# Kernel tuning notes

Measured on AMD Instinct MI355X. Metric: run time of the kernel, lower is better.

Reference implementation:

```python
import jax, jax.numpy as jnp
import numpy as np

N_, CIN, H_, W_ = 2, 128, 240, 320
C_, HEADS, WS, DEPTH, HID, DOUT, NQ = 128, 4, 7, 4, 512, 256, 128

def _ln(x, g, b, eps=1e-5):
    mu = x.mean(-1, keepdims=True)
    var = ((x - mu) ** 2).mean(-1, keepdims=True)
    return (x - mu) / jnp.sqrt(var + eps) * g + b

def setup_inputs() -> dict:
    key = jax.random.key(0)
    ks = jax.random.split(key, 16)
    s = 0.02
    d = {}
    d['x'] = jax.random.normal(ks[0], (N_, CIN, H_, W_), jnp.float32)
    d['conv_w'] = jax.random.normal(ks[1], (C_, CIN), jnp.float32) * s
    d['conv_b'] = jnp.zeros((C_,), jnp.float32)
    d['n1_g'] = jnp.ones((DEPTH, C_), jnp.float32)
    d['n1_b'] = jnp.zeros((DEPTH, C_), jnp.float32)
    d['qkv_w'] = jax.random.normal(ks[2], (DEPTH, 3 * C_, C_), jnp.float32) * s
    d['qkv_b'] = jnp.zeros((DEPTH, 3 * C_), jnp.float32)
    d['proj_w'] = jax.random.normal(ks[3], (DEPTH, C_, C_), jnp.float32) * s
    d['proj_b'] = jnp.zeros((DEPTH, C_), jnp.float32)
    d['n2_g'] = jnp.ones((DEPTH, C_), jnp.float32)
    d['n2_b'] = jnp.zeros((DEPTH, C_), jnp.float32)
    d['fc1_w'] = jax.random.normal(ks[4], (DEPTH, HID, C_), jnp.float32) * s
    d['fc1_b'] = jnp.zeros((DEPTH, HID), jnp.float32)
    d['fc2_w'] = jax.random.normal(ks[5], (DEPTH, C_, HID), jnp.float32) * s
    d['fc2_b'] = jnp.zeros((DEPTH, C_), jnp.float32)
    d['r1_w'] = jax.random.normal(ks[6], (256, C_), jnp.float32) * s
    d['r1_b'] = jnp.zeros((256,), jnp.float32)
    d['r2_w'] = jax.random.normal(ks[7], (256, 256), jnp.float32) * s
    d['r2_b'] = jnp.zeros((256,), jnp.float32)
    d['r3_w'] = jax.random.normal(ks[8], (DOUT, 256), jnp.float32) * s
    d['r3_b'] = jnp.zeros((DOUT,), jnp.float32)
    return d

def _block(t, H, W, n1_g, n1_b, qkv_w, qkv_b, proj_w, proj_b, n2_g, n2_b, fc1_w, fc1_b, fc2_w, fc2_b):
    N, L, C = t.shape
    hd = C // HEADS
    scale = hd ** -0.5
    shortcut = t
    h = _ln(t, n1_g, n1_b).reshape(N, H, W, C)
    pad_h = (-H) % WS
    pad_w = (-W) % WS
    h = jnp.pad(h, ((0, 0), (0, pad_h), (0, pad_w), (0, 0)))
    Hp, Wp = H + pad_h, W + pad_w
    # partition into (num_windows*N, ws*ws, C)
    h = h.reshape(N, Hp // WS, WS, Wp // WS, WS, C).transpose(0, 1, 3, 2, 4, 5).reshape(-1, WS * WS, C)
    B_ = h.shape[0]
    qkv = (h @ qkv_w.T + qkv_b).reshape(B_, WS * WS, 3, HEADS, hd).transpose(2, 0, 3, 1, 4)
    q, k, v = qkv[0], qkv[1], qkv[2]
    attn = jax.nn.softmax(jnp.einsum('bhqd,bhkd->bhqk', q, k) * scale, axis=-1)
    o = jnp.einsum('bhqk,bhkd->bhqd', attn, v).transpose(0, 2, 1, 3).reshape(B_, WS * WS, C)
    o = o @ proj_w.T + proj_b
    # reverse window partition
    o = o.reshape(N, Hp // WS, Wp // WS, WS, WS, C).transpose(0, 1, 3, 2, 4, 5).reshape(N, Hp, Wp, C)[:, :H, :W, :].reshape(N, H * W, C)
    t = shortcut + o
    h2 = _ln(t, n2_g, n2_b)
    m = jax.nn.gelu(h2 @ fc1_w.T + fc1_b, approximate=False) @ fc2_w.T + fc2_b
    return t + m

def reference(x, conv_w, conv_b, n1_g, n1_b, qkv_w, qkv_b, proj_w, proj_b, n2_g, n2_b, fc1_w, fc1_b, fc2_w, fc2_b, r1_w, r1_b, r2_w, r2_b, r3_w, r3_b):
    N, Cin, H, W = x.shape
    xp = jnp.einsum('nchw,ec->nehw', x, conv_w) + conv_b[None, :, None, None]  # (N,C,H,W)
    tokens = xp.reshape(N, C_, H * W).transpose(0, 2, 1)  # (N,HW,C)
    for i in range(DEPTH):
        tokens = _block(tokens, H, W, n1_g[i], n1_b[i], qkv_w[i], qkv_b[i], proj_w[i], proj_b[i], n2_g[i], n2_b[i], fc1_w[i], fc1_b[i], fc2_w[i], fc2_b[i])
    head = tokens.mean(axis=1)  # (N,C)
    queries = tokens[:, :NQ, :]  # (N,NQ,C)
    maps = jnp.einsum('nchw,nqc->nqhw', xp, queries)  # PixelWiseDotProduct
    y = jax.nn.leaky_relu(head @ r1_w.T + r1_b, 0.01)
    y = jax.nn.leaky_relu(y @ r2_w.T + r2_b, 0.01)
    y = y @ r3_w.T + r3_b
    y = jax.nn.relu(y) + 0.1  # norm == 'linear'
    y = y / y.sum(axis=1, keepdims=True)
    return (y, maps)
```

## Files before the change

### kernel.cpp

```cpp
#include <hip/hip_runtime.h>
#include <hip/hip_bf16.h>

typedef __hip_bfloat16 bf16;

static constexpr int Nn = 2, CIN = 128, Hh = 240, Ww = 320, HW = 76800;
static constexpr int Cc = 128, HID = 512, DOUT = 256, WSQ = 49;
static constexpr int NWH = 35, NWW = 46, WPN = NWH * NWW;
static constexpr int NWIN = Nn * WPN;
static constexpr float SCALE = 0.17677669529663687f;

typedef __attribute__((ext_vector_type(8))) short s8;
typedef __attribute__((ext_vector_type(4))) short s4;
typedef __attribute__((ext_vector_type(2))) short s2;
typedef __attribute__((ext_vector_type(4))) float f4;

__device__ __forceinline__ short f2bf(float x) {
  union { bf16 b; short s; } u; u.b = __float2bfloat16(x); return u.s;
}

#define MFMA(a, b, c) __builtin_amdgcn_mfma_f32_16x16x32_bf16((a), (b), (c), 0, 0, 0)

__global__ __launch_bounds__(256) void cast_bf16(const float* __restrict__ src,
                                                 short* __restrict__ dst, int n) {
  const int i = (blockIdx.x * 256 + threadIdx.x) * 4;
  if (i < n) {
    const float4 v = *(const float4*)(src + i);
    s4 o; o[0] = f2bf(v.x); o[1] = f2bf(v.y); o[2] = f2bf(v.z); o[3] = f2bf(v.w);
    *(s4*)(dst + i) = o;
  }
}

__global__ void init_head(float* headbuf) {
  if (threadIdx.x < 256) headbuf[threadIdx.x] = 0.f;
}

__global__ __launch_bounds__(256) void conv_kernel(
    const float* __restrict__ x, const float* __restrict__ conv_w, const float* __restrict__ conv_b,
    float* __restrict__ tok) {
  __shared__ float wlds[128 * 128];
  const int tid = threadIdx.x;
  for (int idx = tid; idx < 16384; idx += 256) {
    const int e = idx & 127, c = idx >> 7;
    wlds[c * 128 + e] = conv_w[e * 128 + c];
  }
  __syncthreads();
  const int n = blockIdx.y;
  const int hw0 = blockIdx.x * 128;
  const int hwi = tid & 63, eg = tid >> 6;
  const float* xn = x + (size_t)n * CIN * HW + hw0 + hwi;
  float acc0[32], acc1[32];
#pragma unroll
  for (int jj = 0; jj < 32; jj++) {
    const float b = conv_b[eg * 32 + jj];
    acc0[jj] = b; acc1[jj] = b;
  }
  for (int c = 0; c < CIN; c++) {
    const float xv0 = xn[(size_t)c * HW];
    const float xv1 = xn[(size_t)c * HW + 64];
    const float* wl = wlds + c * 128 + eg * 32;
#pragma unroll
    for (int jj = 0; jj < 8; jj++) {
      const float4 w4 = *(const float4*)(wl + jj * 4);
      acc0[jj*4+0] = fmaf(w4.x, xv0, acc0[jj*4+0]); acc1[jj*4+0] = fmaf(w4.x, xv1, acc1[jj*4+0]);
      acc0[jj*4+1] = fmaf(w4.y, xv0, acc0[jj*4+1]); acc1[jj*4+1] = fmaf(w4.y, xv1, acc1[jj*4+1]);
      acc0[jj*4+2] = fmaf(w4.z, xv0, acc0[jj*4+2]); acc1[jj*4+2] = fmaf(w4.z, xv1, acc1[jj*4+2]);
      acc0[jj*4+3] = fmaf(w4.w, xv0, acc0[jj*4+3]); acc1[jj*4+3] = fmaf(w4.w, xv1, acc1[jj*4+3]);
    }
  }
  float* tb0 = tok + ((size_t)n * HW + hw0 + hwi) * Cc + eg * 32;
  float* tb1 = tb0 + (size_t)64 * Cc;
#pragma unroll
  for (int jj = 0; jj < 8; jj++) {
    *(float4*)(tb0 + jj * 4) = make_float4(acc0[jj*4], acc0[jj*4+1], acc0[jj*4+2], acc0[jj*4+3]);
    *(float4*)(tb1 + jj * 4) = make_float4(acc1[jj*4], acc1[jj*4+1], acc1[jj*4+2], acc1[jj*4+3]);
  }
}

__global__ __launch_bounds__(256, 2) void attn_kernel(
    float* __restrict__ tok,
    const float* __restrict__ n1_g, const float* __restrict__ n1_b,
    const short* __restrict__ wqkv, const float* __restrict__ qkv_b,
    const short* __restrict__ wproj, const float* __restrict__ proj_b,
    int layer) {
  __shared__ __align__(16) short xwv[9216];
  __shared__ __align__(16) short qkp[4][5120];

  const int tid = threadIdx.x;
  const int w = tid >> 6, lane = tid & 63;
  const int lq = lane >> 4, li = lane & 15;
  const int wi = blockIdx.x;
  const int n = wi / WPN;
  const int r0 = wi % WPN;
  const int wh = r0 / NWW, ww = r0 % NWW;

  const short* wqkv_l = wqkv + (size_t)layer * 384 * 128;
  const short* wproj_l = wproj + (size_t)layer * 128 * 128;

  for (int ti = w; ti < WSQ; ti += 4) {
    const int hh = wh * 7 + ti / 7, wv = ww * 7 + ti % 7;
    const bool valid = (hh < Hh) && (wv < Ww);
    float2 v = make_float2(0.f, 0.f);
    if (valid) v = *(const float2*)(tok + ((size_t)n * HW + hh * Ww + wv) * Cc + 2 * lane);
    float s = v.x + v.y, q = v.x * v.x + v.y * v.y;
#pragma unroll
    for (int m = 1; m < 64; m <<= 1) { s += __shfl_xor(s, m); q += __shfl_xor(q, m); }
    const float mean = s * (1.f / 128.f);
    const float rstd = rsqrtf(fmaxf(q * (1.f / 128.f) - mean * mean, 0.f) + 1e-5f);
    const int c = 2 * lane;
    float o0 = 0.f, o1 = 0.f;
    if (valid) {
      o0 = (v.x - mean) * rstd * n1_g[layer * Cc + c]     + n1_b[layer * Cc + c];
      o1 = (v.y - mean) * rstd * n1_g[layer * Cc + c + 1] + n1_b[layer * Cc + c + 1];
    }
    s2 pk; pk[0] = f2bf(o0); pk[1] = f2bf(o1);
    *(s2*)(xwv + ti * 136 + c) = pk;
  }
  for (int idx = tid; idx < 15 * 136; idx += 256) {
    xwv[(49 + idx / 136) * 136 + (idx % 136)] = 0;
  }
  __syncthreads();

  {
    const int n0 = 64 * w;
    f4 acc[4][4];
#pragma unroll
    for (int mt = 0; mt < 4; mt++)
#pragma unroll
      for (int nt = 0; nt < 4; nt++) acc[mt][nt] = f4{0.f, 0.f, 0.f, 0.f};
    for (int s = 0; s < 4; s++) {
      s8 a[4], b[4];
#pragma unroll
      for (int mt = 0; mt < 4; mt++)
        a[mt] = *(const s8*)(wqkv_l + (n0 + mt * 16 + li) * 128 + s * 32 + lq * 8);
#pragma unroll
      for (int nt = 0; nt < 4; nt++)
        b[nt] = *(const s8*)(xwv + (nt * 16 + li) * 136 + s * 32 + lq * 8);
#pragma unroll
      for (int mt = 0; mt < 4; mt++)
#pragma unroll
        for (int nt = 0; nt < 4; nt++) acc[mt][nt] = MFMA(a[mt], b[nt], acc[mt][nt]);
    }
    const bool isq = (w < 2);
    const float scl = isq ? SCALE : 1.f;
    const int koff = isq ? 0 : 2560;
#pragma unroll
    for (int mt = 0; mt < 4; mt++) {
      const int nbase = n0 + mt * 16 + lq * 4;
      const int hsel = (isq ? nbase : (nbase - 128)) >> 5;
      const int d0 = nbase & 31;
      const float4 bb = *(const float4*)(qkv_b + layer * 384 + nbase);
#pragma unroll
      for (int nt = 0; nt < 4; nt++) {
        const int tokn = nt * 16 + li;
        s4 pk;
        pk[0] = f2bf((acc[mt][nt][0] + bb.x) * scl);
        pk[1] = f2bf((acc[mt][nt][1] + bb.y) * scl);
        pk[2] = f2bf((acc[mt][nt][2] + bb.z) * scl);
        pk[3] = f2bf((acc[mt][nt][3] + bb.w) * scl);
        *(s4*)(qkp[hsel] + koff + tokn * 40 + d0) = pk;
      }
    }
  }

  {
    const int n0v = 32 * w;
    f4 acc2[4][2];
#pragma unroll
    for (int mt = 0; mt < 4; mt++)
#pragma unroll
      for (int nt = 0; nt < 2; nt++) acc2[mt][nt] = f4{0.f, 0.f, 0.f, 0.f};
    for (int s = 0; s < 4; s++) {
      s8 a[4], b[2];
#pragma unroll
      for (int mt = 0; mt < 4; mt++)
        a[mt] = *(const s8*)(xwv + (mt * 16 + li) * 136 + s * 32 + lq * 8);
#pragma unroll
      for (int nt = 0; nt < 2; nt++)
        b[nt] = *(const s8*)(wqkv_l + (256 + n0v + nt * 16 + li) * 128 + s * 32 + lq * 8);
#pragma unroll
      for (int mt = 0; mt < 4; mt++)
#pragma unroll
        for (int nt = 0; nt < 2; nt++) acc2[mt][nt] = MFMA(a[mt], b[nt], acc2[mt][nt]);
    }
    __syncthreads();
#pragma unroll
    for (int nt = 0; nt < 2; nt++) {
      const int d = n0v + nt * 16 + li;
      const float bv = qkv_b[layer * 384 + 256 + d];
#pragma unroll
      for (int mt = 0; mt < 4; mt++) {
        const int m0 = mt * 16 + lq * 4;
        s4 pk;
        pk[0] = f2bf(acc2[mt][nt][0] + bv);
        pk[1] = f2bf(acc2[mt][nt][1] + bv);
        pk[2] = f2bf(acc2[mt][nt][2] + bv);
        pk[3] = f2bf(acc2[mt][nt][3] + bv);
        *(s4*)(xwv + d * 72 + m0) = pk;
      }
    }
  }

  {
    short* qbase = qkp[w];
    short* kbase = qkp[w] + 2560;
    s8 ak[4], bq[4];
#pragma unroll
    for (int kt = 0; kt < 4; kt++) ak[kt] = *(const s8*)(kbase + (kt * 16 + li) * 40 + lq * 8);
#pragma unroll
    for (int qt = 0; qt < 4; qt++) bq[qt] = *(const s8*)(qbase + (qt * 16 + li) * 40 + lq * 8);
    f4 sc[4][4];
#pragma unroll
    for (int kt = 0; kt < 4; kt++)
#pragma unroll
      for (int qt = 0; qt < 4; qt++) sc[kt][qt] = f4{0.f, 0.f, 0.f, 0.f};
#pragma unroll
    for (int kt = 0; kt < 4; kt++)
#pragma unroll
      for (int qt = 0; qt < 4; qt++) sc[kt][qt] = MFMA(ak[kt], bq[qt], sc[kt][qt]);
#pragma unroll
    for (int kt = 0; kt < 4; kt++)
#pragma unroll
      for (int r = 0; r < 4; r++)
        if (kt * 16 + lq * 4 + r >= WSQ) {
#pragma unroll
          for (int qt = 0; qt < 4; qt++) sc[kt][qt][r] = -1e30f;
        }
    float inv[4];
#pragma unroll
    for (int qt = 0; qt < 4; qt++) {
      float m = -1e30f;
#pragma unroll
      for (int kt = 0; kt < 4; kt++)
#pragma unroll
        for (int r = 0; r < 4; r++) m = fmaxf(m, sc[kt][qt][r]);
      m = fmaxf(m, __shfl_xor(m, 16));
      m = fmaxf(m, __shfl_xor(m, 32));
      float ssum = 0.f;
#pragma unroll
      for (int kt = 0; kt < 4; kt++)
#pragma unroll
        for (int r = 0; r < 4; r++) {
          const float e = __expf(sc[kt][qt][r] - m);
          sc[kt][qt][r] = e; ssum += e;
        }
      ssum += __shfl_xor(ssum, 16);
      ssum += __shfl_xor(ssum, 32);
      inv[qt] = 1.f / ssum;
    }
#pragma unroll
    for (int qt = 0; qt < 4; qt++) {
      const int qq = qt * 16 + li;
#pragma unroll
      for (int kt = 0; kt < 4; kt++) {
        s4 pk;
        pk[0] = f2bf(sc[kt][qt][0] * inv[qt]);
        pk[1] = f2bf(sc[kt][qt][1] * inv[qt]);
        pk[2] = f2bf(sc[kt][qt][2] * inv[qt]);
        pk[3] = f2bf(sc[kt][qt][3] * inv[qt]);
        *(s4*)(qbase + qq * 72 + kt * 16 + lq * 4) = pk;
      }
    }
    f4 ov[2][4];
#pragma unroll
    for (int dt = 0; dt < 2; dt++)
#pragma unroll
      for (int qt = 0; qt < 4; qt++) ov[dt][qt] = f4{0.f, 0.f, 0.f, 0.f};
    for (int s = 0; s < 2; s++) {
      s8 av[2], bp[4];
#pragma unroll
      for (int dt = 0; dt < 2; dt++)
        av[dt] = *(const s8*)(xwv + (w * 32 + dt * 16 + li) * 72 + s * 32 + lq * 8);
#pragma unroll
      for (int qt = 0; qt < 4; qt++)
        bp[qt] = *(const s8*)(qbase + (qt * 16 + li) * 72 + s * 32 + lq * 8);
#pragma unroll
      for (int dt = 0; dt < 2; dt++)
#pragma unroll
        for (int qt = 0; qt < 4; qt++) ov[dt][qt] = MFMA(av[dt], bp[qt], ov[dt][qt]);
    }
    short* ohb = qkp[w] + 2560;
#pragma unroll
    for (int dt = 0; dt < 2; dt++) {
      const int dl0 = dt * 16 + lq * 4;
#pragma unroll
      for (int qt = 0; qt < 4; qt++) {
        const int tokn = qt * 16 + li;
        s4 pk;
        pk[0] = f2bf(ov[dt][qt][0]);
        pk[1] = f2bf(ov[dt][qt][1]);
        pk[2] = f2bf(ov[dt][qt][2]);
        pk[3] = f2bf(ov[dt][qt][3]);
        *(s4*)(ohb + tokn * 40 + dl0) = pk;
      }
    }
  }
  __syncthreads();

  {
    const int n0p = 32 * w;
    f4 pa[4][2];
#pragma unroll
    for (int mt = 0; mt < 4; mt++)
#pragma unroll
      for (int nt = 0; nt < 2; nt++) pa[mt][nt] = f4{0.f, 0.f, 0.f, 0.f};
    for (int s = 0; s < 4; s++) {
      s8 ao[4], bw[2];
#pragma unroll
      for (int mt = 0; mt < 4; mt++)
        ao[mt] = *(const s8*)(qkp[s] + 2560 + (mt * 16 + li) * 40 + lq * 8);
#pragma unroll
      for (int nt = 0; nt < 2; nt++)
        bw[nt] = *(const s8*)(wproj_l + (n0p + nt * 16 + li) * 128 + s * 32 + lq * 8);
#pragma unroll
      for (int mt = 0; mt < 4; mt++)
#pragma unroll
        for (int nt = 0; nt < 2; nt++) pa[mt][nt] = MFMA(ao[mt], bw[nt], pa[mt][nt]);
    }
#pragma unroll
    for (int nt = 0; nt < 2; nt++) {
      const int c = n0p + nt * 16 + li;
      const float pb = proj_b[layer * 128 + c];
#pragma unroll
      for (int mt = 0; mt < 4; mt++) {
#pragma unroll
        for (int r = 0; r < 4; r++) {
          const int m = mt * 16 + lq * 4 + r;
          if (m < WSQ) {
            const int hh = wh * 7 + m / 7, wv = ww * 7 + m % 7;
            if (hh < Hh && wv < Ww) {
              float* p = tok + ((size_t)n * HW + hh * Ww + wv) * Cc + c;
              *p += pa[mt][nt][r] + pb;
            }
          }
        }
      }
    }
  }
}

__global__ __launch_bounds__(256, 3) void mlp_kernel(
    float* __restrict__ tok,
    const float* __restrict__ n2_g, const float* __restrict__ n2_b,
    const short* __restrict__ wfc1, const float* __restrict__ fc1_b,
    const short* __restrict__ wfc2, const float* __restrict__ fc2_b,
    int layer) {
  __shared__ __align__(16) short lnb[64 * 136];
  __shared__ __align__(16) short hbuf[2][64 * 136];

  const int tid = threadIdx.x;
  const int w = tid >> 6, lane = tid & 63;
  const int lq = lane >> 4, li = lane & 15;
  const int t0 = blockIdx.x * 64;
  const short* wfc1_l = wfc1 + (size_t)layer * 512 * 128;
  const short* wfc2_l = wfc2 + (size_t)layer * 128 * 512;

#pragma unroll
  for (int i = 0; i < 16; i++) {
    const int tl = w * 16 + i;
    const float2 v = *(const float2*)(tok + (size_t)(t0 + tl) * Cc + 2 * lane);
    float s = v.x + v.y, q = v.x * v.x + v.y * v.y;
#pragma unroll
    for (int m = 1; m < 64; m <<= 1) { s += __shfl_xor(s, m); q += __shfl_xor(q, m); }
    const float mean = s * (1.f / 128.f);
    const float rstd = rsqrtf(fmaxf(q * (1.f / 128.f) - mean * mean, 0.f) + 1e-5f);
    const int c = 2 * lane;
    s2 pk;
    pk[0] = f2bf((v.x - mean) * rstd * n2_g[layer * Cc + c]     + n2_b[layer * Cc + c]);
    pk[1] = f2bf((v.y - mean) * rstd * n2_g[layer * Cc + c + 1] + n2_b[layer * Cc + c + 1]);
    *(s2*)(lnb + tl * 136 + c) = pk;
  }
  __syncthreads();

  f4 acc2[2][4];
#pragma unroll
  for (int mt = 0; mt < 2; mt++)
#pragma unroll
    for (int nt = 0; nt < 4; nt++) acc2[mt][nt] = f4{0.f, 0.f, 0.f, 0.f};
  const int c0 = 32 * w;

  for (int s = 0; s < 4; s++) {
    f4 acc1[2][4];
#pragma unroll
    for (int mt = 0; mt < 2; mt++)
#pragma unroll
      for (int nt = 0; nt < 4; nt++) acc1[mt][nt] = f4{0.f, 0.f, 0.f, 0.f};
    const int hbase = 128 * s + 32 * w;
    for (int kc = 0; kc < 4; kc++) {
      s8 a[2], b[4];
#pragma unroll
      for (int mt = 0; mt < 2; mt++)
        a[mt] = *(const s8*)(wfc1_l + (hbase + mt * 16 + li) * 128 + kc * 32 + lq * 8);
#pragma unroll
      for (int nt = 0; nt < 4; nt++)
        b[nt] = *(const s8*)(lnb + (nt * 16 + li) * 136 + kc * 32 + lq * 8);
#pragma unroll
      for (int mt = 0; mt < 2; mt++)
#pragma unroll
        for (int nt = 0; nt < 4; nt++) acc1[mt][nt] = MFMA(a[mt], b[nt], acc1[mt][nt]);
    }
    short* hb = hbuf[s & 1];
#pragma unroll
    for (int mt = 0; mt < 2; mt++) {
      const int hl0 = 32 * w + mt * 16 + lq * 4;
      const float4 bb = *(const float4*)(fc1_b + layer * HID + 128 * s + hl0);
#pragma unroll
      for (int nt = 0; nt < 4; nt++) {
        const int tokn = nt * 16 + li;
        const float g0 = acc1[mt][nt][0] + bb.x, g1 = acc1[mt][nt][1] + bb.y;
        const float g2 = acc1[mt][nt][2] + bb.z, g3 = acc1[mt][nt][3] + bb.w;
        s4 pk;
        pk[0] = f2bf(0.5f * g0 * (1.f + erff(g0 * 0.70710678118654752f)));
        pk[1] = f2bf(0.5f * g1 * (1.f + erff(g1 * 0.70710678118654752f)));
        pk[2] = f2bf(0.5f * g2 * (1.f + erff(g2 * 0.70710678118654752f)));
        pk[3] = f2bf(0.5f * g3 * (1.f + erff(g3 * 0.70710678118654752f)));
        *(s4*)(hb + tokn * 136 + hl0) = pk;
      }
    }
    __syncthreads();
    for (int kc = 0; kc < 4; kc++) {
      s8 a[2], b[4];
#pragma unroll
      for (int mt = 0; mt < 2; mt++)
        a[mt] = *(const s8*)(wfc2_l + (c0 + mt * 16 + li) * 512 + s * 128 + kc * 32 + lq * 8);
#pragma unroll
      for (int nt = 0; nt < 4; nt++)
        b[nt] = *(const s8*)(hb + (nt * 16 + li) * 136 + kc * 32 + lq * 8);
#pragma unroll
      for (int mt = 0; mt < 2; mt++)
#pragma unroll
        for (int nt = 0; nt < 4; nt++) acc2[mt][nt] = MFMA(a[mt], b[nt], acc2[mt][nt]);
    }
  }

#pragma unroll
  for (int mt = 0; mt < 2; mt++) {
    const int cb = c0 + mt * 16 + lq * 4;
    const float4 bb = *(const float4*)(fc2_b + layer * Cc + cb);
#pragma unroll
    for (int nt = 0; nt < 4; nt++) {
      const int tokn = nt * 16 + li;
      float* p = tok + (size_t)(t0 + tokn) * Cc + cb;
      const float4 g = *(const float4*)p;
      *(float4*)p = make_float4(g.x + acc2[mt][nt][0] + bb.x,
                                g.y + acc2[mt][nt][1] + bb.y,
                                g.z + acc2[mt][nt][2] + bb.z,
                                g.w + acc2[mt][nt][3] + bb.w);
    }
  }
}

__global__ __launch_bounds__(256) void head_kernel(const float* __restrict__ tok,
                                                   float* __restrict__ headbuf) {
  const int n = blockIdx.x >> 6, slice = blockIdx.x & 63;
  const int c = threadIdx.x & 127, half = threadIdx.x >> 7;
  const float* base = tok + ((size_t)n * HW + slice * 1200 + half * 600) * Cc + c;
  float s = 0.f;
  for (int i = 0; i < 600; i++) s += base[(size_t)i * Cc];
  atomicAdd(&headbuf[n * 128 + c], s * (1.f / 76800.f));
}

__global__ __launch_bounds__(256) void y_kernel(
    const float* __restrict__ headbuf,
    const float* __restrict__ r1_w, const float* __restrict__ r1_b,
    const float* __restrict__ r2_w, const float* __restrict__ r2_b,
    const float* __restrict__ r3_w, const float* __restrict__ r3_b,
    float* __restrict__ yout) {
  __shared__ float hb[128], y1[256], y2[256], red4[4];
  const int tid = threadIdx.x;
  const int n = blockIdx.x;
  if (tid < 128) hb[tid] = headbuf[n * 128 + tid];
  __syncthreads();
  {
    float s = r1_b[tid];
    const float* w = r1_w + (size_t)tid * 128;
    for (int c = 0; c < 128; c += 4) {
      const float4 w4 = *(const float4*)(w + c);
      s = fmaf(w4.x, hb[c], s); s = fmaf(w4.y, hb[c+1], s);
      s = fmaf(w4.z, hb[c+2], s); s = fmaf(w4.w, hb[c+3], s);
    }
    y1[tid] = s >= 0.f ? s : 0.01f * s;
  }
  __syncthreads();
  {
    float s = r2_b[tid];
    const float* w = r2_w + (size_t)tid * 256;
    for (int c = 0; c < 256; c += 4) {
      const float4 w4 = *(const float4*)(w + c);
      s = fmaf(w4.x, y1[c], s); s = fmaf(w4.y, y1[c+1], s);
      s = fmaf(w4.z, y1[c+2], s); s = fmaf(w4.w, y1[c+3], s);
    }
    y2[tid] = s >= 0.f ? s : 0.01f * s;
  }
  __syncthreads();
  float v;
  {
    float s = r3_b[tid];
    const float* w = r3_w + (size_t)tid * 256;
    for (int c = 0; c < 256; c += 4) {
      const float4 w4 = *(const float4*)(w + c);
      s = fmaf(w4.x, y2[c], s); s = fmaf(w4.y, y2[c+1], s);
      s = fmaf(w4.z, y2[c+2], s); s = fmaf(w4.w, y2[c+3], s);
    }
    v = (s > 0.f ? s : 0.f) + 0.1f;
  }
  float t = v;
#pragma unroll
  for (int m = 1; m < 64; m <<= 1) t += __shfl_xor(t, m);
  if ((tid & 63) == 0) red4[tid >> 6] = t;
  __syncthreads();
  const float tot = red4[0] + red4[1] + red4[2] + red4[3];
  yout[n * DOUT + tid] = v / tot;
}

__global__ __launch_bounds__(256) void qprep_kernel(
    const float* __restrict__ tok, const float* __restrict__ conv_w, const float* __restrict__ conv_b,
    float* __restrict__ qwx, float* __restrict__ qb) {
  __shared__ float qs[16 * 128];
  const int tid = threadIdx.x;
  const int n = blockIdx.x >> 3, g = blockIdx.x & 7;
  const int q0 = g * 16;
  for (int idx = tid; idx < 2048; idx += 256)
    qs[idx] = tok[((size_t)n * HW + q0 + (idx >> 7)) * Cc + (idx & 127)];
  __syncthreads();
  const int c = tid & 127, half = tid >> 7;
  float acc[8];
#pragma unroll
  for (int j = 0; j < 8; j++) acc[j] = 0.f;
  for (int e = 0; e < 128; e += 4) {
    const float w0 = conv_w[(e + 0) * 128 + c];
    const float w1 = conv_w[(e + 1) * 128 + c];
    const float w2 = conv_w[(e + 2) * 128 + c];
    const float w3 = conv_w[(e + 3) * 128 + c];
#pragma unroll
    for (int j = 0; j < 8; j++) {
      const float4 qv = *(const float4*)(qs + (half * 8 + j) * 128 + e);
      acc[j] = fmaf(qv.x, w0, fmaf(qv.y, w1, fmaf(qv.z, w2, fmaf(qv.w, w3, acc[j]))));
    }
  }
  float* dst = qwx + ((size_t)n * 128 + c) * 128 + q0 + half * 8;
#pragma unroll
  for (int j = 0; j < 8; j++) dst[j] = acc[j];
  if (tid < 16) {
    float s = 0.f;
    for (int e = 0; e < 128; e += 4) {
      const float4 qv = *(const float4*)(qs + tid * 128 + e);
      const float4 bv = *(const float4*)(conv_b + e);
      s = fmaf(qv.x, bv.x, fmaf(qv.y, bv.y, fmaf(qv.z, bv.z, fmaf(qv.w, bv.w, s))));
    }
    qb[n * 128 + q0 + tid] = s;
  }
}

__global__ __launch_bounds__(256) void maps_kernel(
    const float* __restrict__ x, const float* __restrict__ qwx, const float* __restrict__ qb,
    float* __restrict__ mout) {
  __shared__ float qlds[16384];
  const int tid = threadIdx.x;
  const int n = blockIdx.y;
  for (int idx = tid; idx < 16384; idx += 256) qlds[idx] = qwx[(size_t)n * 16384 + idx];
  __syncthreads();
  const int hw0 = blockIdx.x * 128;
  const int hwi = tid & 63, qg = tid >> 6;
  const float* xb = x + (size_t)n * CIN * HW + hw0 + hwi;
  float acc0[32], acc1[32];
#pragma unroll
  for (int jj = 0; jj < 32; jj++) {
    const float b = qb[n * 128 + qg * 32 + jj];
    acc0[jj] = b; acc1[jj] = b;
  }
  for (int c = 0; c < Cc; c++) {
    const float xv0 = xb[(size_t)c * HW];
    const float xv1 = xb[(size_t)c * HW + 64];
    const float* ql = qlds + c * 128 + qg * 32;
#pragma unroll
    for (int jj = 0; jj < 8; jj++) {
      const float4 w4 = *(const float4*)(ql + jj * 4);
      acc0[jj*4+0] = fmaf(w4.x, xv0, acc0[jj*4+0]); acc1[jj*4+0] = fmaf(w4.x, xv1, acc1[jj*4+0]);
      acc0[jj*4+1] = fmaf(w4.y, xv0, acc0[jj*4+1]); acc1[jj*4+1] = fmaf(w4.y, xv1, acc1[jj*4+1]);
      acc0[jj*4+2] = fmaf(w4.z, xv0, acc0[jj*4+2]); acc1[jj*4+2] = fmaf(w4.z, xv1, acc1[jj*4+2]);
      acc0[jj*4+3] = fmaf(w4.w, xv0, acc0[jj*4+3]); acc1[jj*4+3] = fmaf(w4.w, xv1, acc1[jj*4+3]);
    }
  }
  float* mb = mout + ((size_t)n * 128 + qg * 32) * HW + hw0 + hwi;
#pragma unroll
  for (int jj = 0; jj < 32; jj++) {
    mb[(size_t)jj * HW]      = acc0[jj];
    mb[(size_t)jj * HW + 64] = acc1[jj];
  }
}

extern "C" void kernel_launch(void* const* d_in, const int* in_sizes, int n_in,
                              void* d_out, int out_size, void* d_ws, size_t ws_size,
                              hipStream_t stream) {
  const float* x      = (const float*)d_in[0];
  const float* conv_w = (const float*)d_in[1];
  const float* conv_b = (const float*)d_in[2];
  const float* n1_g   = (const float*)d_in[3];
  const float* n1_b   = (const float*)d_in[4];
  const float* qkv_w  = (const float*)d_in[5];
  const float* qkv_b  = (const float*)d_in[6];
  const float* proj_w = (const float*)d_in[7];
  const float* proj_b = (const float*)d_in[8];
  const float* n2_g   = (const float*)d_in[9];
  const float* n2_b   = (const float*)d_in[10];
  const float* fc1_w  = (const float*)d_in[11];
  const float* fc1_b  = (const float*)d_in[12];
  const float* fc2_w  = (const float*)d_in[13];
  const float* fc2_b  = (const float*)d_in[14];
  const float* r1_w   = (const float*)d_in[15];
  const float* r1_b   = (const float*)d_in[16];
  const float* r2_w   = (const float*)d_in[17];
  const float* r2_b   = (const float*)d_in[18];
  const float* r3_w   = (const float*)d_in[19];
  const float* r3_b   = (const float*)d_in[20];

  float* out = (float*)d_out;
  float* tok = out + 512;

  char* ws = (char*)d_ws;
  short* wqkv = (short*)ws;
  short* wproj = (short*)(ws + 393216);
  short* wfc1 = (short*)(ws + 524288);
  short* wfc2 = (short*)(ws + 1048576);
  float* qwx = (float*)(ws + 1572864);
  float* qb = (float*)(ws + 1703936);
  float* headbuf = (float*)(ws + 1704960);

  cast_bf16<<<196608 / 1024, 256, 0, stream>>>(qkv_w, wqkv, 196608);
  cast_bf16<<<65536 / 1024, 256, 0, stream>>>(proj_w, wproj, 65536);
  cast_bf16<<<262144 / 1024, 256, 0, stream>>>(fc1_w, wfc1, 262144);
  cast_bf16<<<262144 / 1024, 256, 0, stream>>>(fc2_w, wfc2, 262144);
  init_head<<<1, 256, 0, stream>>>(headbuf);
  conv_kernel<<<dim3(600, 2), 256, 0, stream>>>(x, conv_w, conv_b, tok);
  for (int l = 0; l < 4; l++) {
    attn_kernel<<<NWIN, 256, 0, stream>>>(tok, n1_g, n1_b, wqkv, qkv_b, wproj, proj_b, l);
    mlp_kernel<<<2400, 256, 0, stream>>>(tok, n2_g, n2_b, wfc1, fc1_b, wfc2, fc2_b, l);
  }
  head_kernel<<<128, 256, 0, stream>>>(tok, headbuf);
  y_kernel<<<2, 256, 0, stream>>>(headbuf, r1_w, r1_b, r2_w, r2_b, r3_w, r3_b, out);
  qprep_kernel<<<16, 256, 0, stream>>>(tok, conv_w, conv_b, qwx, qb);
  maps_kernel<<<dim3(600, 2), 256, 0, stream>>>(x, qwx, qb, out + 512);
}
```

Baseline: 1.599 ms.

## Halve LDS in conv and maps kernels, pretranspose conv weights, prefetch x

```diff
diff --git a/kernel.cpp b/kernel.cpp
--- a/kernel.cpp
+++ b/kernel.cpp
@@ -34,45 +34,60 @@
   if (threadIdx.x < 256) headbuf[threadIdx.x] = 0.f;
 }
 
-__global__ __launch_bounds__(256) void conv_kernel(
-    const float* __restrict__ x, const float* __restrict__ conv_w, const float* __restrict__ conv_b,
+__global__ __launch_bounds__(256) void transp_w(const float* __restrict__ conv_w,
+                                                float* __restrict__ wT) {
+  const int idx = blockIdx.x * 256 + threadIdx.x;
+  const int c = idx >> 7, e = idx & 127;
+  wT[c * 128 + e] = conv_w[e * 128 + c];
+}
+
+__global__ __launch_bounds__(256, 4) void conv_kernel(
+    const float* __restrict__ x, const float* __restrict__ wT, const float* __restrict__ conv_b,
     float* __restrict__ tok) {
-  __shared__ float wlds[128 * 128];
+  __shared__ float wlds[64 * 128];
   const int tid = threadIdx.x;
-  for (int idx = tid; idx < 16384; idx += 256) {
-    const int e = idx & 127, c = idx >> 7;
-    wlds[c * 128 + e] = conv_w[e * 128 + c];
-  }
-  __syncthreads();
+  const int lane = tid & 63, w = tid >> 6;
   const int n = blockIdx.y;
   const int hw0 = blockIdx.x * 128;
-  const int hwi = tid & 63, eg = tid >> 6;
+  const int hwi = 2 * lane;
+  const int e0 = 32 * w;
   const float* xn = x + (size_t)n * CIN * HW + hw0 + hwi;
-  float acc0[32], acc1[32];
-#pragma unroll
-  for (int jj = 0; jj < 32; jj++) {
-    const float b = conv_b[eg * 32 + jj];
-    acc0[jj] = b; acc1[jj] = b;
-  }
-  for (int c = 0; c < CIN; c++) {
-    const float xv0 = xn[(size_t)c * HW];
-    const float xv1 = xn[(size_t)c * HW + 64];
-    const float* wl = wlds + c * 128 + eg * 32;
-#pragma unroll
-    for (int jj = 0; jj < 8; jj++) {
-      const float4 w4 = *(const float4*)(wl + jj * 4);
-      acc0[jj*4+0] = fmaf(w4.x, xv0, acc0[jj*4+0]); acc1[jj*4+0] = fmaf(w4.x, xv1, acc1[jj*4+0]);
-      acc0[jj*4+1] = fmaf(w4.y, xv0, acc0[jj*4+1]); acc1[jj*4+1] = fmaf(w4.y, xv1, acc1[jj*4+1]);
-      acc0[jj*4+2] = fmaf(w4.z, xv0, acc0[jj*4+2]); acc1[jj*4+2] = fmaf(w4.z, xv1, acc1[jj*4+2]);
-      acc0[jj*4+3] = fmaf(w4.w, xv0, acc0[jj*4+3]); acc1[jj*4+3] = fmaf(w4.w, xv1, acc1[jj*4+3]);
-    }
-  }
-  float* tb0 = tok + ((size_t)n * HW + hw0 + hwi) * Cc + eg * 32;
-  float* tb1 = tb0 + (size_t)64 * Cc;
+  float acc[2][32];
 #pragma unroll
   for (int jj = 0; jj < 8; jj++) {
-    *(float4*)(tb0 + jj * 4) = make_float4(acc0[jj*4], acc0[jj*4+1], acc0[jj*4+2], acc0[jj*4+3]);
-    *(float4*)(tb1 + jj * 4) = make_float4(acc1[jj*4], acc1[jj*4+1], acc1[jj*4+2], acc1[jj*4+3]);
+    const float4 b4 = *(const float4*)(conv_b + e0 + jj * 4);
+    acc[0][jj*4+0] = b4.x; acc[1][jj*4+0] = b4.x;
+    acc[0][jj*4+1] = b4.y; acc[1][jj*4+1] = b4.y;
+    acc[0][jj*4+2] = b4.z; acc[1][jj*4+2] = b4.z;
+    acc[0][jj*4+3] = b4.w; acc[1][jj*4+3] = b4.w;
+  }
+  for (int ch = 0; ch < 2; ch++) {
+    if (ch) __syncthreads();
+    for (int idx = tid * 4; idx < 8192; idx += 1024)
+      *(float4*)(wlds + idx) = *(const float4*)(wT + ch * 8192 + idx);
+    __syncthreads();
+    const float* xc = xn + (size_t)(64 * ch) * HW;
+    float2 xv = *(const float2*)(xc);
+    for (int cc = 0; cc < 64; cc++) {
+      const float2 nxt = *(const float2*)(xc + (size_t)(cc < 63 ? cc + 1 : 63) * HW);
+      const float* wl = wlds + cc * 128 + e0;
+#pragma unroll
+      for (int jj = 0; jj < 8; jj++) {
+        const float4 w4 = *(const float4*)(wl + jj * 4);
+        acc[0][jj*4+0] = fmaf(w4.x, xv.x, acc[0][jj*4+0]); acc[1][jj*4+0] = fmaf(w4.x, xv.y, acc[1][jj*4+0]);
+        acc[0][jj*4+1] = fmaf(w4.y, xv.x, acc[0][jj*4+1]); acc[1][jj*4+1] = fmaf(w4.y, xv.y, acc[1][jj*4+1]);
+        acc[0][jj*4+2] = fmaf(w4.z, xv.x, acc[0][jj*4+2]); acc[1][jj*4+2] = fmaf(w4.z, xv.y, acc[1][jj*4+2]);
+        acc[0][jj*4+3] = fmaf(w4.w, xv.x, acc[0][jj*4+3]); acc[1][jj*4+3] = fmaf(w4.w, xv.y, acc[1][jj*4+3]);
+      }
+      xv = nxt;
+    }
+  }
+  float* tb0 = tok + ((size_t)n * HW + hw0 + hwi) * Cc + e0;
+  float* tb1 = tb0 + Cc;
+#pragma unroll
+  for (int jj = 0; jj < 8; jj++) {
+    *(float4*)(tb0 + jj * 4) = make_float4(acc[0][jj*4], acc[0][jj*4+1], acc[0][jj*4+2], acc[0][jj*4+3]);
+    *(float4*)(tb1 + jj * 4) = make_float4(acc[1][jj*4], acc[1][jj*4+1], acc[1][jj*4+2], acc[1][jj*4+3]);
   }
 }
 
@@ -551,41 +566,51 @@
   }
 }
 
-__global__ __launch_bounds__(256) void maps_kernel(
+__global__ __launch_bounds__(256, 4) void maps_kernel(
     const float* __restrict__ x, const float* __restrict__ qwx, const float* __restrict__ qb,
     float* __restrict__ mout) {
-  __shared__ float qlds[16384];
+  __shared__ float qlds[64 * 128];
   const int tid = threadIdx.x;
+  const int lane = tid & 63, w = tid >> 6;
   const int n = blockIdx.y;
-  for (int idx = tid; idx < 16384; idx += 256) qlds[idx] = qwx[(size_t)n * 16384 + idx];
-  __syncthreads();
   const int hw0 = blockIdx.x * 128;
-  const int hwi = tid & 63, qg = tid >> 6;
-  const float* xb = x + (size_t)n * CIN * HW + hw0 + hwi;
-  float acc0[32], acc1[32];
+  const int hwi = 2 * lane;
+  const int q0 = 32 * w;
+  const float* xn = x + (size_t)n * CIN * HW + hw0 + hwi;
+  float acc[2][32];
+#pragma unroll
+  for (int jj = 0; jj < 8; jj++) {
+    const float4 b4 = *(const float4*)(qb + n * 128 + q0 + jj * 4);
+    acc[0][jj*4+0] = b4.x; acc[1][jj*4+0] = b4.x;
+    acc[0][jj*4+1] = b4.y; acc[1][jj*4+1] = b4.y;
+    acc[0][jj*4+2] = b4.z; acc[1][jj*4+2] = b4.z;
+    acc[0][jj*4+3] = b4.w; acc[1][jj*4+3] = b4.w;
+  }
+  for (int ch = 0; ch < 2; ch++) {
+    if (ch) __syncthreads();
+    for (int idx = tid * 4; idx < 8192; idx += 1024)
+      *(float4*)(qlds + idx) = *(const float4*)(qwx + (size_t)n * 16384 + ch * 8192 + idx);
+    __syncthreads();
+    const float* xc = xn + (size_t)(64 * ch) * HW;
+    float2 xv = *(const float2*)(xc);
+    for (int cc = 0; cc < 64; cc++) {
+      const float2 nxt = *(const float2*)(xc + (size_t)(cc < 63 ? cc + 1 : 63) * HW);
+      const float* ql = qlds + cc * 128 + q0;
+#pragma unroll
+      for (int jj = 0; jj < 8; jj++) {
+        const float4 w4 = *(const float4*)(ql + jj * 4);
+        acc[0][jj*4+0] = fmaf(w4.x, xv.x, acc[0][jj*4+0]); acc[1][jj*4+0] = fmaf(w4.x, xv.y, acc[1][jj*4+0]);
+        acc[0][jj*4+1] = fmaf(w4.y, xv.x, acc[0][jj*4+1]); acc[1][jj*4+1] = fmaf(w4.y, xv.y, acc[1][jj*4+1]);
+        acc[0][jj*4+2] = fmaf(w4.z, xv.x, acc[0][jj*4+2]); acc[1][jj*4+2] = fmaf(w4.z, xv.y, acc[1][jj*4+2]);
+        acc[0][jj*4+3] = fmaf(w4.w, xv.x, acc[0][jj*4+3]); acc[1][jj*4+3] = fmaf(w4.w, xv.y, acc[1][jj*4+3]);
+      }
+      xv = nxt;
+    }
+  }
+  float* mb = mout + ((size_t)n * 128 + q0) * HW + hw0 + hwi;
 #pragma unroll
   for (int jj = 0; jj < 32; jj++) {
-    const float b = qb[n * 128 + qg * 32 + jj];
-    acc0[jj] = b; acc1[jj] = b;
-  }
-  for (int c = 0; c < Cc; c++) {
-    const float xv0 = xb[(size_t)c * HW];
-    const float xv1 = xb[(size_t)c * HW + 64];
-    const float* ql = qlds + c * 128 + qg * 32;
-#pragma unroll
-    for (int jj = 0; jj < 8; jj++) {
-      const float4 w4 = *(const float4*)(ql + jj * 4);
-      acc0[jj*4+0] = fmaf(w4.x, xv0, acc0[jj*4+0]); acc1[jj*4+0] = fmaf(w4.x, xv1, acc1[jj*4+0]);
-      acc0[jj*4+1] = fmaf(w4.y, xv0, acc0[jj*4+1]); acc1[jj*4+1] = fmaf(w4.y, xv1, acc1[jj*4+1]);
-      acc0[jj*4+2] = fmaf(w4.z, xv0, acc0[jj*4+2]); acc1[jj*4+2] = fmaf(w4.z, xv1, acc1[jj*4+2]);
-      acc0[jj*4+3] = fmaf(w4.w, xv0, acc0[jj*4+3]); acc1[jj*4+3] = fmaf(w4.w, xv1, acc1[jj*4+3]);
-    }
-  }
-  float* mb = mout + ((size_t)n * 128 + qg * 32) * HW + hw0 + hwi;
-#pragma unroll
-  for (int jj = 0; jj < 32; jj++) {
-    mb[(size_t)jj * HW]      = acc0[jj];
-    mb[(size_t)jj * HW + 64] = acc1[jj];
+    *(float2*)(mb + (size_t)jj * HW) = make_float2(acc[0][jj], acc[1][jj]);
   }
 }
 
@@ -625,13 +650,15 @@
   float* qwx = (float*)(ws + 1572864);
   float* qb = (float*)(ws + 1703936);
   float* headbuf = (float*)(ws + 1704960);
+  float* wconvT = qwx;
 
   cast_bf16<<<196608 / 1024, 256, 0, stream>>>(qkv_w, wqkv, 196608);
   cast_bf16<<<65536 / 1024, 256, 0, stream>>>(proj_w, wproj, 65536);
   cast_bf16<<<262144 / 1024, 256, 0, stream>>>(fc1_w, wfc1, 262144);
   cast_bf16<<<262144 / 1024, 256, 0, stream>>>(fc2_w, wfc2, 262144);
   init_head<<<1, 256, 0, stream>>>(headbuf);
-  conv_kernel<<<dim3(600, 2), 256, 0, stream>>>(x, conv_w, conv_b, tok);
+  transp_w<<<64, 256, 0, stream>>>(conv_w, wconvT);
+  conv_kernel<<<dim3(600, 2), 256, 0, stream>>>(x, wconvT, conv_b, tok);
   for (int l = 0; l < 4; l++) {
     attn_kernel<<<NWIN, 256, 0, stream>>>(tok, n1_g, n1_b, wqkv, qkv_b, wproj, proj_b, l);
     mlp_kernel<<<2400, 256, 0, stream>>>(tok, n2_g, n2_b, wfc1, fc1_b, wfc2, fc2_b, l);
```

Result: slower. 2.024 ms (+26.5%).
